# Optimization experiments

Hardware: AMD Instinct MI355X
Metric: run time of the kernel (lower is better)

The kernel has to match this reference:

```python
import jax, jax.numpy as jnp
import numpy as np

B = 32768
D_IN = 512      # input_dim == dict_dim (forced by the STE add)
HID = 512       # hard-coded hidden width of linear1
D = 512         # dict_dim / embedding_dim
P = 8           # per_factor_dict_size: number of codebooks / MLP branches
K = 10          # num_factor: codebook size (rows per embedding table)
COMMIT = 0.25


def setup_inputs() -> dict:
    key = jax.random.key(0)
    ks = jax.random.split(key, 7)
    s1 = 1.0 / np.sqrt(D_IN)
    s2 = 1.0 / np.sqrt(HID)
    return {
        "inputs": jax.random.normal(ks[0], (B, D_IN), jnp.float32),
        "W1": jax.random.uniform(ks[1], (P, HID, D_IN), jnp.float32, -s1, s1),
        "b1": jax.random.uniform(ks[2], (P, HID), jnp.float32, -s1, s1),
        "W2": jax.random.uniform(ks[3], (P, D, HID), jnp.float32, -s2, s2),
        "b2": jax.random.uniform(ks[4], (P, D), jnp.float32, -s2, s2),
        # embedding init: uniform(-1/num_factor, 1/num_factor)
        "E": jax.random.uniform(ks[5], (P, K, D), jnp.float32, -1.0 / K, 1.0 / K),
        "label_gen": jax.random.randint(ks[6], (B,), 0, K, jnp.int64),
    }


def reference(inputs, W1, b1, W2, b2, E, label_gen):
    sg = jax.lax.stop_gradient
    # P parallel 2-layer MLPs: [P, B, D]
    h = jax.nn.relu(jnp.einsum("bd,phd->pbh", inputs, W1) + b1[:, None, :])
    z = jnp.einsum("pbh,peh->pbe", h, W2) + b2[:, None, :]
    # squared-distance expansion per codebook: [P, B, K]
    distances = (
        jnp.sum(z * z, axis=-1, keepdims=True)
        + jnp.sum(E * E, axis=-1)[:, None, :]
        - 2.0 * jnp.einsum("pbd,pkd->pbk", z, E)
    )
    ave_distances = jnp.mean(distances, axis=0)          # [B, K]
    idx = jnp.argmin(ave_distances, axis=1)              # [B]
    # one-hot @ E[p] then mean over p == mean codebook gathered at idx
    Emean = jnp.mean(E, axis=0)                          # [K, D]
    vq = Emean[idx]                                      # [B, D]
    vq_z = inputs + sg(vq - inputs)                      # straight-through
    # all_vq_z[j] = mean_p E[p, j]; losses vs every code row: [K, B]
    diff1 = Emean[:, None, :] - sg(inputs)[None, :, :]   # [K, B, D]
    diff2 = sg(Emean)[:, None, :] - inputs[None, :, :]
    all_vq_loss = jnp.sum(diff1 * diff1, axis=-1) + COMMIT * jnp.sum(diff2 * diff2, axis=-1)
    all_vq_z = inputs[None, :, :] + sg(Emean[:, None, :] - inputs[None, :, :])  # [K, B, D]
    changed_vq_z = Emean[label_gen]                      # [B, D]
    return (vq_z, distances, all_vq_z, all_vq_loss, changed_vq_z)
```

## Files before the change

kernel.cpp:

```cpp
#include <hip/hip_runtime.h>
#include <stdint.h>

typedef _Float16 f16;
typedef _Float16 f16x8 __attribute__((ext_vector_type(8)));
typedef float f32x4 __attribute__((ext_vector_type(4)));

#define B_ROWS 32768
#define DIM 512
#define NP 8
#define NK 10

typedef __attribute__((address_space(3))) unsigned int lds_u32;
typedef __attribute__((address_space(1))) const unsigned int gbl_u32;

__device__ __forceinline__ void gload_lds16(const void* g, void* l) {
  __builtin_amdgcn_global_load_lds((gbl_u32*)(uintptr_t)g, (lds_u32*)(uintptr_t)l, 16, 0, 0);
}


__global__ void split_kernel(const float* __restrict__ src, f16* __restrict__ hi,
                             f16* __restrict__ lo, int n) {
  int i = blockIdx.x * 256 + threadIdx.x;
  int stride = gridDim.x * 256;
  for (; i < n; i += stride) {
    float v = src[i];
    f16 h = (f16)v;
    hi[i] = h;
    lo[i] = (f16)(v - (float)h);
  }
}

__global__ void emean_kernel(const float* __restrict__ E, float* __restrict__ Emean) {
  int i = blockIdx.x * 256 + threadIdx.x;
  if (i < NK * DIM) {
    float s = 0.f;
#pragma unroll
    for (int p = 0; p < NP; ++p) s += E[p * NK * DIM + i];
    Emean[i] = s * 0.125f;
  }
}

__global__ void enorm_kernel(const float* __restrict__ E, const float* __restrict__ Emean,
                             float* __restrict__ E2, float* __restrict__ E2m) {
  int bid = blockIdx.x;
  const float* src = (bid < 80) ? (E + (size_t)bid * DIM) : (Emean + (size_t)(bid - 80) * DIM);
  int lane = threadIdx.x;
  float s = 0.f;
  for (int i = lane; i < DIM; i += 64) {
    float v = src[i];
    s = fmaf(v, v, s);
  }
#pragma unroll
  for (int m = 1; m < 64; m <<= 1) s += __shfl_xor(s, m, 64);
  if (lane == 0) {
    if (bid < 80) E2[bid] = s;
    else E2m[bid - 80] = s;
  }
}

__global__ __launch_bounds__(512) void etilde_kernel(const float* __restrict__ W2,
                                                     const float* __restrict__ b2,
                                                     const float* __restrict__ E,
                                                     float* __restrict__ Et,
                                                     float* __restrict__ c_) {
  const int p = blockIdx.x / NK, k = blockIdx.x % NK;
  const int h = threadIdx.x;
  __shared__ float Er[512];
  __shared__ float red[8];
  Er[h] = E[((size_t)p * NK + k) * DIM + h];
  __syncthreads();
  const float* Wp = W2 + (size_t)p * DIM * DIM;
  float s = 0.f;
#pragma unroll 8
  for (int d = 0; d < DIM; ++d) s = fmaf(Wp[(size_t)d * DIM + h], Er[d], s);
  Et[((size_t)p * NK + k) * DIM + h] = s;
  float t = b2[p * DIM + h] * Er[h];
#pragma unroll
  for (int m = 1; m < 64; m <<= 1) t += __shfl_xor(t, m, 64);
  if ((h & 63) == 0) red[h >> 6] = t;
  __syncthreads();
  if (h == 0) {
    float cc = 0.f;
#pragma unroll
    for (int i = 0; i < 8; ++i) cc += red[i];
    c_[p * NK + k] = cc;
  }
}


template <int EPI, int NBN, int NPROD>
__global__ __launch_bounds__(256) void gemmA(
    const f16* __restrict__ Ah_, const f16* __restrict__ Al_, int lda, int apitch,
    const f16* __restrict__ Bh_, const f16* __restrict__ Bl_, int bpitch,
    const float* __restrict__ bias_, int bias_pitch,
    f16* __restrict__ Oh, f16* __restrict__ Ol, int ldo,
    float* __restrict__ part2) {
  __shared__ f16 smem[32768];
  const int tid = threadIdx.x;
  const int lane = tid & 63;
  const int wave = tid >> 6;
  const int wr = wave >> 1, wc = wave & 1;
  const int p = blockIdx.z;

  const int q8 = gridDim.x >> 3;
  const int bid = blockIdx.x;
  const int swz = (bid & 7) * q8 + (bid >> 3);
  const int bm = swz / NBN, bn = swz % NBN;
  const int m0 = bm * 128, n0 = bn * 128;

  const f16* Ahp = Ah_ + (size_t)p * apitch;
  const f16* Alp = Al_ + (size_t)p * apitch;
  const f16* Bhp = Bh_ + (size_t)p * bpitch;
  const f16* Blp = Bl_ + (size_t)p * bpitch;

  const int NT = (NPROD == 3) ? 24 : 8;

  f32x4 acc[4][4] = {};

  auto stage = [&](int buf, int t) {
    const f16* As;
    const f16* Bs;
    int k0;
    if (NPROD == 3) {
      int pr = t % 3;
      As = (pr == 2) ? Alp : Ahp;
      Bs = (pr == 1) ? Blp : Bhp;
      k0 = (t / 3) * 64;
    } else {
      As = Ahp;
      Bs = Bhp;
      k0 = t * 64;
    }
    f16* sA = smem + buf * 16384;
    f16* sB = sA + 8192;
#pragma unroll
    for (int j = 0; j < 4; ++j) {
      int r = j * 32 + (tid >> 3);
      int c = ((tid & 7) ^ (r & 7)) * 8;
      gload_lds16(As + (size_t)(m0 + r) * lda + k0 + c, sA + j * 2048 + tid * 8);
      gload_lds16(Bs + (size_t)(n0 + r) * 512 + k0 + c, sB + j * 2048 + tid * 8);
    }
  };

  stage(0, 0);
  __syncthreads();

  const int g = lane >> 4, rl = lane & 15;

  for (int s = 0; s < NT; ++s) {
    int nx = s + 1;
    if (nx < NT) stage(nx & 1, nx);
    const char* sA = (const char*)(smem + (s & 1) * 16384);
    const char* sB = sA + 16384;
    f16x8 af[4][2], bf[4][2];
#pragma unroll
    for (int i = 0; i < 4; ++i) {
      int ra = wr * 64 + i * 16 + rl;
      int rb = wc * 64 + i * 16 + rl;
#pragma unroll
      for (int kk = 0; kk < 2; ++kk) {
        int cb = kk * 64 + g * 16;
        af[i][kk] = *(const f16x8*)(sA + ra * 128 + (cb ^ ((ra & 7) << 4)));
        bf[i][kk] = *(const f16x8*)(sB + rb * 128 + (cb ^ ((rb & 7) << 4)));
      }
    }
#pragma unroll
    for (int i = 0; i < 4; ++i)
#pragma unroll
      for (int jn = 0; jn < 4; ++jn)
#pragma unroll
        for (int kk = 0; kk < 2; ++kk)
          acc[i][jn] = __builtin_amdgcn_mfma_f32_16x16x32_f16(af[i][kk], bf[jn][kk], acc[i][jn], 0, 0, 0);
    __syncthreads();
  }

  if (EPI == 0) {
#pragma unroll
    for (int jn = 0; jn < 4; ++jn) {
      int cg = n0 + wc * 64 + jn * 16 + rl;
      float bv = bias_[cg];
#pragma unroll
      for (int i = 0; i < 4; ++i) {
        int r0 = m0 + wr * 64 + i * 16 + g * 4;
#pragma unroll
        for (int r = 0; r < 4; ++r) {
          float z = acc[i][jn][r] + bv;
          z = fmaxf(z, 0.f);
          f16 h = (f16)z;
          size_t off = (size_t)(r0 + r) * ldo + cg;
          Oh[off] = h;
          Ol[off] = (f16)(z - (float)h);
        }
      }
    }
  } else {
    const float* bp = bias_ + (size_t)p * bias_pitch;
    float bvals[4];
#pragma unroll
    for (int jn = 0; jn < 4; ++jn) bvals[jn] = bp[n0 + wc * 64 + jn * 16 + rl];
    const int ch = bn * 2 + wc;
    float* pb = part2 + (size_t)(p * 8 + ch) * B_ROWS;
#pragma unroll
    for (int i = 0; i < 4; ++i) {
#pragma unroll
      for (int r = 0; r < 4; ++r) {
        float q = 0.f;
#pragma unroll
        for (int jn = 0; jn < 4; ++jn) {
          float z = acc[i][jn][r] + bvals[jn];
          q = fmaf(z, z, q);
        }
#pragma unroll
        for (int m = 1; m < 16; m <<= 1) q += __shfl_xor(q, m, 64);
        if (rl == 0) pb[m0 + wr * 64 + i * 16 + g * 4 + r] = q;
      }
    }
  }
}


__global__ __launch_bounds__(256) void dots_kernel(const f16* __restrict__ Hh,
                                                   const f16* __restrict__ Hl,
                                                   const float* __restrict__ Et,
                                                   const float* __restrict__ c_,
                                                   float* __restrict__ g) {
  const int p = blockIdx.y;
  const int lane = threadIdx.x & 63, wave = threadIdx.x >> 6;
  float4 et[NK][2];
#pragma unroll
  for (int k = 0; k < NK; ++k) {
    const float* ep = Et + ((size_t)p * NK + k) * DIM + lane * 8;
    et[k][0] = *(const float4*)ep;
    et[k][1] = *(const float4*)(ep + 4);
  }
  float cv[NK];
#pragma unroll
  for (int k = 0; k < NK; ++k) cv[k] = c_[p * NK + k];
  const int r0 = blockIdx.x * 128 + wave * 32;
  for (int rr = 0; rr < 32; ++rr) {
    int row = r0 + rr;
    const f16* hhp = Hh + (size_t)row * 4096 + p * DIM + lane * 8;
    const f16* hlp = Hl + (size_t)row * 4096 + p * DIM + lane * 8;
    f16x8 hh = *(const f16x8*)hhp;
    f16x8 hl = *(const f16x8*)hlp;
    float h[8];
#pragma unroll
    for (int j = 0; j < 8; ++j) h[j] = (float)hh[j] + (float)hl[j];
    float d[NK];
#pragma unroll
    for (int k = 0; k < NK; ++k) {
      float s = h[0] * et[k][0].x;
      s = fmaf(h[1], et[k][0].y, s);
      s = fmaf(h[2], et[k][0].z, s);
      s = fmaf(h[3], et[k][0].w, s);
      s = fmaf(h[4], et[k][1].x, s);
      s = fmaf(h[5], et[k][1].y, s);
      s = fmaf(h[6], et[k][1].z, s);
      s = fmaf(h[7], et[k][1].w, s);
      d[k] = s;
    }
#pragma unroll
    for (int m = 1; m < 64; m <<= 1)
#pragma unroll
      for (int k = 0; k < NK; ++k) d[k] += __shfl_xor(d[k], m, 64);
    float* gp = g + ((size_t)p * B_ROWS + row) * NK;
#pragma unroll
    for (int k = 0; k < NK; ++k)
      if (lane == k) gp[k] = d[k] + cv[k];
  }
}


__global__ __launch_bounds__(256) void final_kernel(
    const float* __restrict__ X, const float* __restrict__ part2,
    const float* __restrict__ g, const float* __restrict__ E2,
    const float* __restrict__ Emean, const float* __restrict__ E2m,
    const int* __restrict__ label, float* __restrict__ vq_z,
    float* __restrict__ dist, float* __restrict__ loss, float* __restrict__ changed) {
  __shared__ float Em[NK * DIM];
  __shared__ float e2s[NK];
  for (int i = threadIdx.x; i < NK * DIM; i += 256) Em[i] = Emean[i];
  if (threadIdx.x < NK) e2s[threadIdx.x] = E2m[threadIdx.x];
  __syncthreads();
  const int lane = threadIdx.x & 63, wave = threadIdx.x >> 6;
  const int pl = lane & 7, kh = lane >> 3;
  for (int rr = 0; rr < 4; ++rr) {
    int b = blockIdx.x * 16 + wave * 4 + rr;
    float zq = part2[(size_t)(pl * 8 + kh) * B_ROWS + b];
    zq += __shfl_xor(zq, 8, 64);
    zq += __shfl_xor(zq, 16, 64);
    zq += __shfl_xor(zq, 32, 64);
    float g0 = g[((size_t)pl * B_ROWS + b) * NK + kh];
    float g1 = (lane < 16) ? g[((size_t)pl * B_ROWS + b) * NK + 8 + kh] : 0.f;
    float dv0 = zq + E2[pl * NK + kh] - 2.f * g0;
    float dv1 = zq + E2[pl * NK + 8 + kh] - 2.f * g1;
    dist[((size_t)pl * B_ROWS + b) * NK + kh] = dv0;
    if (lane < 16) dist[((size_t)pl * B_ROWS + b) * NK + 8 + kh] = dv1;
    float v0 = dv0, v1 = dv1;
#pragma unroll
    for (int m = 1; m < 8; m <<= 1) {
      v0 += __shfl_xor(v0, m, 64);
      v1 += __shfl_xor(v1, m, 64);
    }
    float a[NK];
#pragma unroll
    for (int k = 0; k < 8; ++k) a[k] = __shfl(v0, k * 8, 64);
    a[8] = __shfl(v1, 0, 64);
    a[9] = __shfl(v1, 8, 64);
    int idx = 0;
    float mn = a[0];
#pragma unroll
    for (int k = 1; k < NK; ++k) {
      if (a[k] < mn) { mn = a[k]; idx = k; }
    }
    const float* xr = X + (size_t)b * DIM;
    float sx = 0.f, dx[NK] = {};
#pragma unroll
    for (int j = 0; j < 8; ++j) {
      float x = xr[j * 64 + lane];
      sx = fmaf(x, x, sx);
#pragma unroll
      for (int k = 0; k < NK; ++k) dx[k] = fmaf(x, Em[k * DIM + j * 64 + lane], dx[k]);
    }
#pragma unroll
    for (int m = 1; m < 64; m <<= 1) {
      sx += __shfl_xor(sx, m, 64);
#pragma unroll
      for (int k = 0; k < NK; ++k) dx[k] += __shfl_xor(dx[k], m, 64);
    }
    if (lane == 0) {
#pragma unroll
      for (int k = 0; k < NK; ++k)
        loss[(size_t)k * B_ROWS + b] = 1.25f * (sx - 2.f * dx[k] + e2s[k]);
    }
    int lab = label[b];
#pragma unroll
    for (int j = 0; j < 8; ++j) {
      int c = j * 64 + lane;
      vq_z[(size_t)b * DIM + c] = Em[idx * DIM + c];
      changed[(size_t)b * DIM + c] = Em[lab * DIM + c];
    }
  }
}


__global__ void bcast_kernel(const float* __restrict__ Emean, float4* __restrict__ out) {
  const float4* Em4 = (const float4*)Emean;
  size_t n = (size_t)NK * B_ROWS * (DIM / 4);
  for (size_t i = (size_t)blockIdx.x * blockDim.x + threadIdx.x; i < n;
       i += (size_t)gridDim.x * blockDim.x) {
    size_t kb = i >> 7;
    int d4 = (int)(i & 127);
    int k = (int)(kb >> 15);
    out[i] = Em4[k * 128 + d4];
  }
}


extern "C" void kernel_launch(void* const* d_in, const int* in_sizes, int n_in,
                              void* d_out, int out_size, void* d_ws, size_t ws_size,
                              hipStream_t stream) {
  const float* X = (const float*)d_in[0];
  const float* W1 = (const float*)d_in[1];
  const float* b1 = (const float*)d_in[2];
  const float* W2 = (const float*)d_in[3];
  const float* b2 = (const float*)d_in[4];
  const float* E = (const float*)d_in[5];
  const int* lab = (const int*)d_in[6];
  float* out = (float*)d_out;

  float* vq_z = out;
  float* dist = out + 16777216;
  float* avz = out + 16777216 + 2621440;
  float* loss = avz + 167772160;
  float* chg = loss + 327680;

  f16* Xh = (f16*)vq_z;
  f16* Xl = Xh + 16777216;
  f16* Hh = (f16*)avz;
  f16* Hl = Hh + 134217728;
  float* part2 = avz + 134217728;
  float* gbuf = part2 + 2097152;

  char* w = (char*)d_ws;
  f16* W1h = (f16*)w; w += 4194304;
  f16* W1l = (f16*)w; w += 4194304;
  f16* W2h = (f16*)w; w += 4194304;
  f16* W2l = (f16*)w; w += 4194304;
  float* Emean = (float*)w; w += NK * DIM * 4;
  float* E2 = (float*)w; w += 512;
  float* E2m = (float*)w; w += 256;
  float* Et = (float*)w; w += NP * NK * DIM * 4;
  float* c_ = (float*)w; w += 512;

  split_kernel<<<2048, 256, 0, stream>>>(X, Xh, Xl, 16777216);
  split_kernel<<<512, 256, 0, stream>>>(W1, W1h, W1l, 2097152);
  split_kernel<<<512, 256, 0, stream>>>(W2, W2h, W2l, 2097152);
  emean_kernel<<<20, 256, 0, stream>>>(E, Emean);
  enorm_kernel<<<90, 64, 0, stream>>>(E, Emean, E2, E2m);
  etilde_kernel<<<80, 512, 0, stream>>>(W2, b2, E, Et, c_);

  gemmA<0, 32, 3><<<dim3(8192, 1, 1), 256, 0, stream>>>(
      Xh, Xl, 512, 0, W1h, W1l, 0, b1, 0, Hh, Hl, 4096, nullptr);
  gemmA<1, 4, 1><<<dim3(1024, 1, NP), 256, 0, stream>>>(
      Hh, Hh, 4096, 512, W2h, W2h, 262144, b2, 512, nullptr, nullptr, 0, part2);

  dots_kernel<<<dim3(256, NP), 256, 0, stream>>>(Hh, Hl, Et, c_, gbuf);
  final_kernel<<<2048, 256, 0, stream>>>(X, part2, gbuf, E2, Emean, E2m, lab,
                                         vq_z, dist, loss, chg);
  bcast_kernel<<<4096, 256, 0, stream>>>(Emean, (float4*)avz);
}
```

Measured before the change: 1.249 ms.

## Move codebook dot products onto MFMA and group-swizzle first GEMM tiles

Replaces the scalar FMA plus shuffle-reduction dots kernel with an MFMA kernel. It stages the hidden activations (hi/lo fp16 halves) into swizzled LDS through direct global-to-LDS loads, and multiplies them against a padded fp16 hi/lo image of the projected codebook built by a new pack kernel, using three split-precision products. Separately, the first GEMM's block-to-tile mapping is regrouped into bands of 8 row tiles per column, aiming for better L2 reuse of the activation tiles. The MFMA path pads K from 10 to 16 and drops the lo×lo term, which slightly changes the rounding of the distances.

```diff
diff --git a/kernel.cpp b/kernel.cpp
--- a/kernel.cpp
+++ b/kernel.cpp
@@ -87,8 +87,22 @@
   }
 }
 
-
-template <int EPI, int NBN, int NPROD>
+__global__ void epack_kernel(const float* __restrict__ Et, f16* __restrict__ EimgH,
+                             f16* __restrict__ EimgL) {
+  int i = blockIdx.x * 256 + threadIdx.x;
+  const int tot = NP * 16 * 520;
+  if (i >= tot) return;
+  int p = i / (16 * 520);
+  int rem = i % (16 * 520);
+  int k = rem / 520, h = rem % 520;
+  float v = (k < NK && h < DIM) ? Et[((size_t)p * NK + k) * DIM + h] : 0.f;
+  f16 hi = (f16)v;
+  EimgH[i] = hi;
+  EimgL[i] = (f16)(v - (float)hi);
+}
+
+
+template <int EPI, int NBN, int NPROD, int GRP>
 __global__ __launch_bounds__(256) void gemmA(
     const f16* __restrict__ Ah_, const f16* __restrict__ Al_, int lda, int apitch,
     const f16* __restrict__ Bh_, const f16* __restrict__ Bl_, int bpitch,
@@ -105,7 +119,10 @@
   const int q8 = gridDim.x >> 3;
   const int bid = blockIdx.x;
   const int swz = (bid & 7) * q8 + (bid >> 3);
-  const int bm = swz / NBN, bn = swz % NBN;
+  const int band = swz / (GRP * NBN);
+  const int r_ = swz % (GRP * NBN);
+  const int bm = band * GRP + (r_ % GRP);
+  const int bn = r_ / GRP;
   const int m0 = bm * 128, n0 = bn * 128;
 
   const f16* Ahp = Ah_ + (size_t)p * apitch;
@@ -219,54 +236,81 @@
 }
 
 
-__global__ __launch_bounds__(256) void dots_kernel(const f16* __restrict__ Hh,
-                                                   const f16* __restrict__ Hl,
-                                                   const float* __restrict__ Et,
-                                                   const float* __restrict__ c_,
-                                                   float* __restrict__ g) {
+__global__ __launch_bounds__(256) void dots_mfma(const f16* __restrict__ Hh,
+                                                 const f16* __restrict__ Hl,
+                                                 const f16* __restrict__ EimgH,
+                                                 const f16* __restrict__ EimgL,
+                                                 const float* __restrict__ c_,
+                                                 float* __restrict__ gout) {
+  __shared__ f16 sH[8192];
+  __shared__ f16 sL[8192];
+  __shared__ f16 sEh[16 * 520];
+  __shared__ f16 sEl[16 * 520];
+  const int tid = threadIdx.x;
+  const int lane = tid & 63, wave = tid >> 6;
   const int p = blockIdx.y;
-  const int lane = threadIdx.x & 63, wave = threadIdx.x >> 6;
-  float4 et[NK][2];
-#pragma unroll
-  for (int k = 0; k < NK; ++k) {
-    const float* ep = Et + ((size_t)p * NK + k) * DIM + lane * 8;
-    et[k][0] = *(const float4*)ep;
-    et[k][1] = *(const float4*)(ep + 4);
-  }
-  float cv[NK];
-#pragma unroll
-  for (int k = 0; k < NK; ++k) cv[k] = c_[p * NK + k];
-  const int r0 = blockIdx.x * 128 + wave * 32;
-  for (int rr = 0; rr < 32; ++rr) {
-    int row = r0 + rr;
-    const f16* hhp = Hh + (size_t)row * 4096 + p * DIM + lane * 8;
-    const f16* hlp = Hl + (size_t)row * 4096 + p * DIM + lane * 8;
-    f16x8 hh = *(const f16x8*)hhp;
-    f16x8 hl = *(const f16x8*)hlp;
-    float h[8];
-#pragma unroll
-    for (int j = 0; j < 8; ++j) h[j] = (float)hh[j] + (float)hl[j];
-    float d[NK];
-#pragma unroll
-    for (int k = 0; k < NK; ++k) {
-      float s = h[0] * et[k][0].x;
-      s = fmaf(h[1], et[k][0].y, s);
-      s = fmaf(h[2], et[k][0].z, s);
-      s = fmaf(h[3], et[k][0].w, s);
-      s = fmaf(h[4], et[k][1].x, s);
-      s = fmaf(h[5], et[k][1].y, s);
-      s = fmaf(h[6], et[k][1].z, s);
-      s = fmaf(h[7], et[k][1].w, s);
-      d[k] = s;
-    }
-#pragma unroll
-    for (int m = 1; m < 64; m <<= 1)
-#pragma unroll
-      for (int k = 0; k < NK; ++k) d[k] += __shfl_xor(d[k], m, 64);
-    float* gp = g + ((size_t)p * B_ROWS + row) * NK;
-#pragma unroll
-    for (int k = 0; k < NK; ++k)
-      if (lane == k) gp[k] = d[k] + cv[k];
+  const int r0 = blockIdx.x * 128;
+  {
+    const uint32_t* ih = (const uint32_t*)(EimgH + (size_t)p * 16 * 520);
+    const uint32_t* il = (const uint32_t*)(EimgL + (size_t)p * 16 * 520);
+    uint32_t* oh = (uint32_t*)sEh;
+    uint32_t* ol = (uint32_t*)sEl;
+    for (int i = tid; i < 16 * 520 / 2; i += 256) {
+      oh[i] = ih[i];
+      ol[i] = il[i];
+    }
+  }
+  const int gq = lane >> 4, rl = lane & 15;
+  f32x4 acc[2] = {};
+  for (int t = 0; t < 8; ++t) {
+    __syncthreads();
+#pragma unroll
+    for (int j = 0; j < 4; ++j) {
+      int r = j * 32 + (tid >> 3);
+      int c = ((tid & 7) ^ (r & 7)) * 8;
+      gload_lds16(Hh + (size_t)(r0 + r) * 4096 + p * DIM + t * 64 + c, sH + j * 2048 + tid * 8);
+      gload_lds16(Hl + (size_t)(r0 + r) * 4096 + p * DIM + t * 64 + c, sL + j * 2048 + tid * 8);
+    }
+    __syncthreads();
+    const char* bh = (const char*)sH;
+    const char* bl = (const char*)sL;
+    const char* eh = (const char*)sEh;
+    const char* el = (const char*)sEl;
+    f16x8 ah[2][2], al[2][2], beh[2], bel[2];
+#pragma unroll
+    for (int mf = 0; mf < 2; ++mf) {
+      int ra = wave * 32 + mf * 16 + rl;
+#pragma unroll
+      for (int kk = 0; kk < 2; ++kk) {
+        int cb = kk * 64 + gq * 16;
+        ah[mf][kk] = *(const f16x8*)(bh + ra * 128 + (cb ^ ((ra & 7) << 4)));
+        al[mf][kk] = *(const f16x8*)(bl + ra * 128 + (cb ^ ((ra & 7) << 4)));
+      }
+    }
+#pragma unroll
+    for (int kk = 0; kk < 2; ++kk) {
+      int cb = t * 128 + kk * 64 + gq * 16;
+      beh[kk] = *(const f16x8*)(eh + rl * 1040 + cb);
+      bel[kk] = *(const f16x8*)(el + rl * 1040 + cb);
+    }
+#pragma unroll
+    for (int mf = 0; mf < 2; ++mf)
+#pragma unroll
+      for (int kk = 0; kk < 2; ++kk) {
+        acc[mf] = __builtin_amdgcn_mfma_f32_16x16x32_f16(ah[mf][kk], beh[kk], acc[mf], 0, 0, 0);
+        acc[mf] = __builtin_amdgcn_mfma_f32_16x16x32_f16(ah[mf][kk], bel[kk], acc[mf], 0, 0, 0);
+        acc[mf] = __builtin_amdgcn_mfma_f32_16x16x32_f16(al[mf][kk], beh[kk], acc[mf], 0, 0, 0);
+      }
+  }
+  if (rl < NK) {
+    float cv = c_[p * NK + rl];
+#pragma unroll
+    for (int mf = 0; mf < 2; ++mf)
+#pragma unroll
+      for (int r = 0; r < 4; ++r) {
+        int row = r0 + wave * 32 + mf * 16 + gq * 4 + r;
+        gout[((size_t)p * B_ROWS + row) * NK + rl] = acc[mf][r] + cv;
+      }
   }
 }
 
@@ -392,6 +436,8 @@
   float* E2m = (float*)w; w += 256;
   float* Et = (float*)w; w += NP * NK * DIM * 4;
   float* c_ = (float*)w; w += 512;
+  f16* EimgH = (f16*)w; w += NP * 16 * 520 * 2;
+  f16* EimgL = (f16*)w; w += NP * 16 * 520 * 2;
 
   split_kernel<<<2048, 256, 0, stream>>>(X, Xh, Xl, 16777216);
   split_kernel<<<512, 256, 0, stream>>>(W1, W1h, W1l, 2097152);
@@ -399,13 +445,14 @@
   emean_kernel<<<20, 256, 0, stream>>>(E, Emean);
   enorm_kernel<<<90, 64, 0, stream>>>(E, Emean, E2, E2m);
   etilde_kernel<<<80, 512, 0, stream>>>(W2, b2, E, Et, c_);
-
-  gemmA<0, 32, 3><<<dim3(8192, 1, 1), 256, 0, stream>>>(
+  epack_kernel<<<260, 256, 0, stream>>>(Et, EimgH, EimgL);
+
+  gemmA<0, 32, 3, 8><<<dim3(8192, 1, 1), 256, 0, stream>>>(
       Xh, Xl, 512, 0, W1h, W1l, 0, b1, 0, Hh, Hl, 4096, nullptr);
-  gemmA<1, 4, 1><<<dim3(1024, 1, NP), 256, 0, stream>>>(
+  gemmA<1, 4, 1, 1><<<dim3(1024, 1, NP), 256, 0, stream>>>(
       Hh, Hh, 4096, 512, W2h, W2h, 262144, b2, 512, nullptr, nullptr, 0, part2);
 
-  dots_kernel<<<dim3(256, NP), 256, 0, stream>>>(Hh, Hl, Et, c_, gbuf);
+  dots_mfma<<<dim3(256, NP), 256, 0, stream>>>(Hh, Hl, EimgH, EimgL, c_, gbuf);
   final_kernel<<<2048, 256, 0, stream>>>(X, part2, gbuf, E2, Emean, E2m, lab,
                                          vq_z, dist, loss, chg);
   bcast_kernel<<<4096, 256, 0, stream>>>(Emean, (float4*)avz);
```

Measured after the change: 1.140 ms. -8.7%, faster.

## Fuse codebook dot products into first GEMM epilogue and drop H low-part

Applied to the files above, without the earlier changes.

The first GEMM epilogue now computes each row's partial dot products against the projected codebooks Et directly from the fp32 activations. It writes per-column-chunk partials that final_kernel sums, which removes the separate dots_kernel and its reread of H. The H low-half buffer and W2 low split are dropped, and H stores are staged through LDS for coalesced 16-byte writes. A grouped tile swizzle is added for L2 reuse. The epilogue adds register pressure and extra partial-buffer traffic.

```diff
diff --git a/kernel.cpp b/kernel.cpp
--- a/kernel.cpp
+++ b/kernel.cpp
@@ -28,6 +28,12 @@
     hi[i] = h;
     lo[i] = (f16)(v - (float)h);
   }
+}
+
+__global__ void splith_kernel(const float* __restrict__ src, f16* __restrict__ hi, int n) {
+  int i = blockIdx.x * 256 + threadIdx.x;
+  int stride = gridDim.x * 256;
+  for (; i < n; i += stride) hi[i] = (f16)src[i];
 }
 
 __global__ void emean_kernel(const float* __restrict__ E, float* __restrict__ Emean) {
@@ -88,13 +94,13 @@
 }
 
 
-template <int EPI, int NBN, int NPROD>
+template <int EPI, int NBN, int NPROD, int GRP>
 __global__ __launch_bounds__(256) void gemmA(
     const f16* __restrict__ Ah_, const f16* __restrict__ Al_, int lda, int apitch,
     const f16* __restrict__ Bh_, const f16* __restrict__ Bl_, int bpitch,
     const float* __restrict__ bias_, int bias_pitch,
-    f16* __restrict__ Oh, f16* __restrict__ Ol, int ldo,
-    float* __restrict__ part2) {
+    f16* __restrict__ Oh, int ldo,
+    float* __restrict__ part2, const float* __restrict__ Et_, float* __restrict__ gpart) {
   __shared__ f16 smem[32768];
   const int tid = threadIdx.x;
   const int lane = tid & 63;
@@ -105,7 +111,10 @@
   const int q8 = gridDim.x >> 3;
   const int bid = blockIdx.x;
   const int swz = (bid & 7) * q8 + (bid >> 3);
-  const int bm = swz / NBN, bn = swz % NBN;
+  const int band = swz / (GRP * NBN);
+  const int r_ = swz % (GRP * NBN);
+  const int bm = band * GRP + (r_ % GRP);
+  const int bn = r_ / GRP;
   const int m0 = bm * 128, n0 = bn * 128;
 
   const f16* Ahp = Ah_ + (size_t)p * apitch;
@@ -175,23 +184,53 @@
   }
 
   if (EPI == 0) {
+    const int pp = bn >> 2, cc = bn & 3;
+    float bv[4];
+#pragma unroll
+    for (int jn = 0; jn < 4; ++jn) bv[jn] = bias_[n0 + wc * 64 + jn * 16 + rl];
+    float ev[NK][4];
 #pragma unroll
     for (int jn = 0; jn < 4; ++jn) {
-      int cg = n0 + wc * 64 + jn * 16 + rl;
-      float bv = bias_[cg];
-#pragma unroll
-      for (int i = 0; i < 4; ++i) {
-        int r0 = m0 + wr * 64 + i * 16 + g * 4;
-#pragma unroll
-        for (int r = 0; r < 4; ++r) {
-          float z = acc[i][jn][r] + bv;
-          z = fmaxf(z, 0.f);
-          f16 h = (f16)z;
-          size_t off = (size_t)(r0 + r) * ldo + cg;
-          Oh[off] = h;
-          Ol[off] = (f16)(z - (float)h);
+      int col = cc * 128 + wc * 64 + jn * 16 + rl;
+      const float* ep = Et_ + (size_t)pp * NK * DIM + col;
+#pragma unroll
+      for (int k = 0; k < NK; ++k) ev[k][jn] = ep[k * DIM];
+    }
+    f16* sOut = smem;
+    float* pgb = gpart + (size_t)(pp * 8 + cc * 2 + wc) * B_ROWS * 12;
+#pragma unroll
+    for (int i = 0; i < 4; ++i) {
+#pragma unroll
+      for (int r = 0; r < 4; ++r) {
+        int row = wr * 64 + i * 16 + g * 4 + r;
+        float qv[NK];
+#pragma unroll
+        for (int k = 0; k < NK; ++k) qv[k] = 0.f;
+#pragma unroll
+        for (int jn = 0; jn < 4; ++jn) {
+          float z = fmaxf(acc[i][jn][r] + bv[jn], 0.f);
+          sOut[row * 128 + wc * 64 + jn * 16 + rl] = (f16)z;
+#pragma unroll
+          for (int k = 0; k < NK; ++k) qv[k] = fmaf(z, ev[k][jn], qv[k]);
+        }
+#pragma unroll
+        for (int m = 1; m < 16; m <<= 1)
+#pragma unroll
+          for (int k = 0; k < NK; ++k) qv[k] += __shfl_xor(qv[k], m, 64);
+        if (rl == 0) {
+          float* o = pgb + (size_t)(m0 + row) * 12;
+          *(float4*)o = make_float4(qv[0], qv[1], qv[2], qv[3]);
+          *(float4*)(o + 4) = make_float4(qv[4], qv[5], qv[6], qv[7]);
+          *(float2*)(o + 8) = make_float2(qv[8], qv[9]);
         }
       }
+    }
+    __syncthreads();
+#pragma unroll
+    for (int j = 0; j < 8; ++j) {
+      int row = j * 16 + (tid >> 4);
+      f16x8 vv = *(const f16x8*)(sOut + row * 128 + (tid & 15) * 8);
+      *(f16x8*)(Oh + (size_t)(m0 + row) * ldo + n0 + (tid & 15) * 8) = vv;
     }
   } else {
     const float* bp = bias_ + (size_t)p * bias_pitch;
@@ -219,64 +258,13 @@
 }
 
 
-__global__ __launch_bounds__(256) void dots_kernel(const f16* __restrict__ Hh,
-                                                   const f16* __restrict__ Hl,
-                                                   const float* __restrict__ Et,
-                                                   const float* __restrict__ c_,
-                                                   float* __restrict__ g) {
-  const int p = blockIdx.y;
-  const int lane = threadIdx.x & 63, wave = threadIdx.x >> 6;
-  float4 et[NK][2];
-#pragma unroll
-  for (int k = 0; k < NK; ++k) {
-    const float* ep = Et + ((size_t)p * NK + k) * DIM + lane * 8;
-    et[k][0] = *(const float4*)ep;
-    et[k][1] = *(const float4*)(ep + 4);
-  }
-  float cv[NK];
-#pragma unroll
-  for (int k = 0; k < NK; ++k) cv[k] = c_[p * NK + k];
-  const int r0 = blockIdx.x * 128 + wave * 32;
-  for (int rr = 0; rr < 32; ++rr) {
-    int row = r0 + rr;
-    const f16* hhp = Hh + (size_t)row * 4096 + p * DIM + lane * 8;
-    const f16* hlp = Hl + (size_t)row * 4096 + p * DIM + lane * 8;
-    f16x8 hh = *(const f16x8*)hhp;
-    f16x8 hl = *(const f16x8*)hlp;
-    float h[8];
-#pragma unroll
-    for (int j = 0; j < 8; ++j) h[j] = (float)hh[j] + (float)hl[j];
-    float d[NK];
-#pragma unroll
-    for (int k = 0; k < NK; ++k) {
-      float s = h[0] * et[k][0].x;
-      s = fmaf(h[1], et[k][0].y, s);
-      s = fmaf(h[2], et[k][0].z, s);
-      s = fmaf(h[3], et[k][0].w, s);
-      s = fmaf(h[4], et[k][1].x, s);
-      s = fmaf(h[5], et[k][1].y, s);
-      s = fmaf(h[6], et[k][1].z, s);
-      s = fmaf(h[7], et[k][1].w, s);
-      d[k] = s;
-    }
-#pragma unroll
-    for (int m = 1; m < 64; m <<= 1)
-#pragma unroll
-      for (int k = 0; k < NK; ++k) d[k] += __shfl_xor(d[k], m, 64);
-    float* gp = g + ((size_t)p * B_ROWS + row) * NK;
-#pragma unroll
-    for (int k = 0; k < NK; ++k)
-      if (lane == k) gp[k] = d[k] + cv[k];
-  }
-}
-
-
 __global__ __launch_bounds__(256) void final_kernel(
     const float* __restrict__ X, const float* __restrict__ part2,
-    const float* __restrict__ g, const float* __restrict__ E2,
-    const float* __restrict__ Emean, const float* __restrict__ E2m,
-    const int* __restrict__ label, float* __restrict__ vq_z,
-    float* __restrict__ dist, float* __restrict__ loss, float* __restrict__ changed) {
+    const float* __restrict__ gpart, const float* __restrict__ c_,
+    const float* __restrict__ E2, const float* __restrict__ Emean,
+    const float* __restrict__ E2m, const int* __restrict__ label,
+    float* __restrict__ vq_z, float* __restrict__ dist,
+    float* __restrict__ loss, float* __restrict__ changed) {
   __shared__ float Em[NK * DIM];
   __shared__ float e2s[NK];
   for (int i = threadIdx.x; i < NK * DIM; i += 256) Em[i] = Emean[i];
@@ -290,10 +278,16 @@
     zq += __shfl_xor(zq, 8, 64);
     zq += __shfl_xor(zq, 16, 64);
     zq += __shfl_xor(zq, 32, 64);
-    float g0 = g[((size_t)pl * B_ROWS + b) * NK + kh];
-    float g1 = (lane < 16) ? g[((size_t)pl * B_ROWS + b) * NK + 8 + kh] : 0.f;
-    float dv0 = zq + E2[pl * NK + kh] - 2.f * g0;
-    float dv1 = zq + E2[pl * NK + 8 + kh] - 2.f * g1;
+    size_t gb = ((size_t)(pl * 8) * B_ROWS + b) * 12;
+    float g0 = 0.f, g1 = 0.f;
+#pragma unroll
+    for (int ch = 0; ch < 8; ++ch) {
+      const float* q = gpart + gb + (size_t)ch * B_ROWS * 12;
+      g0 += q[kh];
+      if (lane < 16) g1 += q[8 + kh];
+    }
+    float dv0 = zq + E2[pl * NK + kh] - 2.f * (g0 + c_[pl * NK + kh]);
+    float dv1 = (lane < 16) ? zq + E2[pl * NK + 8 + kh] - 2.f * (g1 + c_[pl * NK + 8 + kh]) : 0.f;
     dist[((size_t)pl * B_ROWS + b) * NK + kh] = dv0;
     if (lane < 16) dist[((size_t)pl * B_ROWS + b) * NK + 8 + kh] = dv1;
     float v0 = dv0, v1 = dv1;
@@ -378,15 +372,13 @@
   f16* Xh = (f16*)vq_z;
   f16* Xl = Xh + 16777216;
   f16* Hh = (f16*)avz;
-  f16* Hl = Hh + 134217728;
-  float* part2 = avz + 134217728;
-  float* gbuf = part2 + 2097152;
+  float* part2 = avz + 67108864;
+  float* gpart = part2 + 2097152;
 
   char* w = (char*)d_ws;
   f16* W1h = (f16*)w; w += 4194304;
   f16* W1l = (f16*)w; w += 4194304;
   f16* W2h = (f16*)w; w += 4194304;
-  f16* W2l = (f16*)w; w += 4194304;
   float* Emean = (float*)w; w += NK * DIM * 4;
   float* E2 = (float*)w; w += 512;
   float* E2m = (float*)w; w += 256;
@@ -395,18 +387,17 @@
 
   split_kernel<<<2048, 256, 0, stream>>>(X, Xh, Xl, 16777216);
   split_kernel<<<512, 256, 0, stream>>>(W1, W1h, W1l, 2097152);
-  split_kernel<<<512, 256, 0, stream>>>(W2, W2h, W2l, 2097152);
+  splith_kernel<<<512, 256, 0, stream>>>(W2, W2h, 2097152);
   emean_kernel<<<20, 256, 0, stream>>>(E, Emean);
   enorm_kernel<<<90, 64, 0, stream>>>(E, Emean, E2, E2m);
   etilde_kernel<<<80, 512, 0, stream>>>(W2, b2, E, Et, c_);
 
-  gemmA<0, 32, 3><<<dim3(8192, 1, 1), 256, 0, stream>>>(
-      Xh, Xl, 512, 0, W1h, W1l, 0, b1, 0, Hh, Hl, 4096, nullptr);
-  gemmA<1, 4, 1><<<dim3(1024, 1, NP), 256, 0, stream>>>(
-      Hh, Hh, 4096, 512, W2h, W2h, 262144, b2, 512, nullptr, nullptr, 0, part2);
-
-  dots_kernel<<<dim3(256, NP), 256, 0, stream>>>(Hh, Hl, Et, c_, gbuf);
-  final_kernel<<<2048, 256, 0, stream>>>(X, part2, gbuf, E2, Emean, E2m, lab,
+  gemmA<0, 32, 3, 8><<<dim3(8192, 1, 1), 256, 0, stream>>>(
+      Xh, Xl, 512, 0, W1h, W1l, 0, b1, 0, Hh, 4096, nullptr, Et, gpart);
+  gemmA<1, 4, 1, 1><<<dim3(1024, 1, NP), 256, 0, stream>>>(
+      Hh, Hh, 4096, 512, W2h, W2h, 262144, b2, 512, nullptr, 0, part2, nullptr, nullptr);
+
+  final_kernel<<<2048, 256, 0, stream>>>(X, part2, gpart, c_, E2, Emean, E2m, lab,
                                          vq_z, dist, loss, chg);
   bcast_kernel<<<4096, 256, 0, stream>>>(Emean, (float4*)avz);
 }
```

Result: faster. 1.199 ms (-4.0%).
